# Kernel tuning notes

Hardware: AMD Instinct MI355X
Metric: run time of the kernel (lower is better)

## Reference

```python
import jax, jax.numpy as jnp
import numpy as np

NEG_SLOPE = 0.3

def capped_lrelu(x):
    # clamp(LeakyReLU_0.3(x), max=1)
    return jnp.minimum(jnp.where(x >= 0, x, NEG_SLOPE * x), 1.0)

def setup_inputs() -> dict:
    key = jax.random.key(0)
    ks = jax.random.split(key, 8)
    B, T, V, H, O = 64, 512, 512, 256, 512
    s = 1.0 / np.sqrt(H)
    return {
        "sentence": jax.random.normal(ks[0], (B, T, V), dtype=jnp.float32),
        "prev_state": jnp.zeros((1, B, H), dtype=jnp.float32),
        "W_ih": jax.random.normal(ks[1], (H, V), dtype=jnp.float32) * s,
        "b_ih": jax.random.normal(ks[2], (H,), dtype=jnp.float32) * s,
        "W_hh": jax.random.normal(ks[3], (H, H), dtype=jnp.float32) * s,
        "b_hh": jax.random.normal(ks[4], (H,), dtype=jnp.float32) * s,
        "W_out": jax.random.normal(ks[5], (O, H), dtype=jnp.float32) * s,
        "b_out": jax.random.normal(ks[6], (O,), dtype=jnp.float32) * s,
    }

def reference(sentence, prev_state, W_ih, b_ih, W_hh, b_hh, W_out, b_out):
    # nn.RNN(nonlinearity='relu'), batch_first, n_layers=1:
    #   h_t = relu(x_t @ W_ih^T + b_ih + h_{t-1} @ W_hh^T + b_hh)
    # Precompute input projections for all timesteps, scan the recurrence.
    x_proj = jnp.einsum('btv,hv->bth', sentence, W_ih) + b_ih  # [B,T,H]
    x_proj_t = jnp.swapaxes(x_proj, 0, 1)                      # [T,B,H]
    h0 = prev_state[0]                                         # [B,H]

    def step(h, xt):
        h_new = jax.nn.relu(xt + h @ W_hh.T + b_hh)
        return h_new, h_new

    h_last, out_seq = jax.lax.scan(step, h0, x_proj_t)         # [T,B,H]
    out_seq = jnp.swapaxes(out_seq, 0, 1)                      # [B,T,H]

    hidden_activ = capped_lrelu(out_seq)
    tags = jax.nn.sigmoid(jnp.einsum('bth,oh->bto', hidden_activ, W_out) + b_out)
    h_n = h_last[None]                                         # [1,B,H]
    return tags, h_n
```

## Files before the change

kernel.cpp:

```cpp
#include <hip/hip_runtime.h>
#include <hip/hip_bf16.h>


typedef __attribute__((ext_vector_type(8))) _Float16 half8;
typedef __attribute__((ext_vector_type(4))) _Float16 half4;
typedef __attribute__((ext_vector_type(4))) float   floatx4;

__device__ __forceinline__ void lds_barrier() {
    asm volatile("s_waitcnt lgkmcnt(0)\n\ts_barrier" ::: "memory");
}

__global__ void conv_f32_f16(const float* __restrict__ in, _Float16* __restrict__ out, int n4) {
    int idx = blockIdx.x * blockDim.x + threadIdx.x;
    if (idx >= n4) return;
    float4 v = ((const float4*)in)[idx];
    half4 h = { (_Float16)v.x, (_Float16)v.y, (_Float16)v.z, (_Float16)v.w };
    ((half4*)out)[idx] = h;
}

__global__ __launch_bounds__(256) void gemm1_xproj(const float* __restrict__ A,
                                                   const _Float16* __restrict__ Bw,
                                                   const float* __restrict__ b_ih,
                                                   const float* __restrict__ b_hh,
                                                   float* __restrict__ C) {
    const int K = 512, N = 256;
    int wave = threadIdx.x >> 6;
    int lane = threadIdx.x & 63;
    int row  = lane & 15;
    int quad = lane >> 4;
    int m0 = blockIdx.x * 64 + wave * 16;

    floatx4 acc[16];
#pragma unroll
    for (int i = 0; i < 16; i++) acc[i] = (floatx4){0.f, 0.f, 0.f, 0.f};

    const float* pa = A + (size_t)(m0 + row) * K + quad * 8;
    for (int k0 = 0; k0 < K; k0 += 32) {
        float4 a0 = *(const float4*)(pa + k0);
        float4 a1 = *(const float4*)(pa + k0 + 4);
        half8 a = { (_Float16)a0.x, (_Float16)a0.y, (_Float16)a0.z, (_Float16)a0.w,
                    (_Float16)a1.x, (_Float16)a1.y, (_Float16)a1.z, (_Float16)a1.w };
#pragma unroll
        for (int nt = 0; nt < 16; nt++) {
            const _Float16* pb = Bw + (size_t)(nt * 16 + row) * K + quad * 8 + k0;
            half8 b = *(const half8*)pb;
            acc[nt] = __builtin_amdgcn_mfma_f32_16x16x32_f16(a, b, acc[nt], 0, 0, 0);
        }
    }
#pragma unroll
    for (int nt = 0; nt < 16; nt++) {
        int n = nt * 16 + row;
        float bn = b_ih[n] + b_hh[n];
#pragma unroll
        for (int r = 0; r < 4; r++) {
            int m = m0 + quad * 4 + r;
            C[(size_t)m * N + n] = acc[nt][r] + bn;
        }
    }
}

__global__ __launch_bounds__(512, 2) void rnn_recur(const float* __restrict__ xp,
                                                    const float* __restrict__ h0,
                                                    const float* __restrict__ W_hh,
                                                    _Float16* __restrict__ hid,
                                                    float* __restrict__ h_n) {
    const int Hh = 256, T = 512, LD = 264;
    int b0   = blockIdx.x * 16;
    int wave = threadIdx.x >> 6;
    int lane = threadIdx.x & 63;
    int c    = lane & 15;
    int q    = lane >> 4;

    half8 wf[2][8];
#pragma unroll
    for (int nt = 0; nt < 2; nt++) {
        int n = (wave * 2 + nt) * 16 + c;
        const float* wr = W_hh + (size_t)n * Hh + q * 8;
#pragma unroll
        for (int kt = 0; kt < 8; kt++) {
            float4 x0 = *(const float4*)(wr + kt * 32);
            float4 x1 = *(const float4*)(wr + kt * 32 + 4);
            wf[nt][kt] = (half8){ (_Float16)x0.x, (_Float16)x0.y, (_Float16)x0.z, (_Float16)x0.w,
                                  (_Float16)x1.x, (_Float16)x1.y, (_Float16)x1.z, (_Float16)x1.w };
        }
    }

    __shared__ _Float16 hb[2][16][LD];
    for (int idx = threadIdx.x; idx < 16 * 256; idx += 512) {
        int m = idx >> 8, k = idx & 255;
        hb[0][m][k] = (_Float16)h0[(size_t)(b0 + m) * Hh + k];
    }
    __syncthreads();

    const float* xpb = xp + (size_t)(b0 + c) * T * Hh;
    _Float16* hidb = hid + (size_t)(b0 + c) * T * Hh;

    int noff[2];
#pragma unroll
    for (int nt = 0; nt < 2; nt++) noff[nt] = (wave * 2 + nt) * 16 + q * 4;

    float4 xq0[2], xq1[2];
#pragma unroll
    for (int nt = 0; nt < 2; nt++) {
        xq0[nt] = *(const float4*)(xpb + (size_t)0 * Hh + noff[nt]);
        xq1[nt] = *(const float4*)(xpb + (size_t)1 * Hh + noff[nt]);
    }

    auto do_step = [&](int t, float4 (&xq)[2]) {
        const _Float16* hr = &hb[t & 1][0][0];
        floatx4 aA0 = {0.f,0.f,0.f,0.f}, aA1 = {0.f,0.f,0.f,0.f};
        floatx4 aB0 = {0.f,0.f,0.f,0.f}, aB1 = {0.f,0.f,0.f,0.f};
#pragma unroll
        for (int kt = 0; kt < 4; kt++) {
            half8 hfA = *(const half8*)(hr + c * LD + kt * 32 + q * 8);
            half8 hfB = *(const half8*)(hr + c * LD + (kt + 4) * 32 + q * 8);
            aA0 = __builtin_amdgcn_mfma_f32_16x16x32_f16(wf[0][kt],     hfA, aA0, 0, 0, 0);
            aB0 = __builtin_amdgcn_mfma_f32_16x16x32_f16(wf[0][kt + 4], hfB, aB0, 0, 0, 0);
            aA1 = __builtin_amdgcn_mfma_f32_16x16x32_f16(wf[1][kt],     hfA, aA1, 0, 0, 0);
            aB1 = __builtin_amdgcn_mfma_f32_16x16x32_f16(wf[1][kt + 4], hfB, aB1, 0, 0, 0);
        }
        floatx4 acc[2];
        acc[0] = aA0 + aB0;
        acc[1] = aA1 + aB1;

        _Float16* hw = &hb[(t + 1) & 1][0][0];
#pragma unroll
        for (int nt = 0; nt < 2; nt++) {
            float v0 = fmaxf(acc[nt][0] + xq[nt].x, 0.f);
            float v1 = fmaxf(acc[nt][1] + xq[nt].y, 0.f);
            float v2 = fmaxf(acc[nt][2] + xq[nt].z, 0.f);
            float v3 = fmaxf(acc[nt][3] + xq[nt].w, 0.f);
            half4 hv = { (_Float16)v0, (_Float16)v1, (_Float16)v2, (_Float16)v3 };
            *(half4*)(hw + c * LD + noff[nt]) = hv;
            half4 hc = { (_Float16)fminf(v0, 1.f), (_Float16)fminf(v1, 1.f),
                         (_Float16)fminf(v2, 1.f), (_Float16)fminf(v3, 1.f) };
            *(half4*)(hidb + (size_t)t * Hh + noff[nt]) = hc;
            if (t == T - 1) {
                float4 hn = { v0, v1, v2, v3 };
                *(float4*)(h_n + (size_t)(b0 + c) * Hh + noff[nt]) = hn;
            }
        }
        int tp = (t + 2 < T) ? t + 2 : T - 1;
#pragma unroll
        for (int nt = 0; nt < 2; nt++)
            xq[nt] = *(const float4*)(xpb + (size_t)tp * Hh + noff[nt]);

        lds_barrier();
    };

    for (int t = 0; t < T; t += 2) {
        do_step(t,     xq0);
        do_step(t + 1, xq1);
    }
}

__global__ __launch_bounds__(256) void gemm3_tags(const _Float16* __restrict__ A,
                                                  const _Float16* __restrict__ Bw,
                                                  const float* __restrict__ bias,
                                                  float* __restrict__ C) {
    const int K = 256, N = 512;
    int wave = threadIdx.x >> 6;
    int lane = threadIdx.x & 63;
    int row  = lane & 15;
    int quad = lane >> 4;
    int m0 = blockIdx.x * 64 + wave * 16;
    int n_base = blockIdx.y * 256;

    floatx4 acc[16];
#pragma unroll
    for (int i = 0; i < 16; i++) acc[i] = (floatx4){0.f, 0.f, 0.f, 0.f};

    const _Float16* pa = A + (size_t)(m0 + row) * K + quad * 8;
    for (int k0 = 0; k0 < K; k0 += 32) {
        half8 a = *(const half8*)(pa + k0);
#pragma unroll
        for (int nt = 0; nt < 16; nt++) {
            const _Float16* pb = Bw + (size_t)(n_base + nt * 16 + row) * K + quad * 8 + k0;
            half8 b = *(const half8*)pb;
            acc[nt] = __builtin_amdgcn_mfma_f32_16x16x32_f16(a, b, acc[nt], 0, 0, 0);
        }
    }
#pragma unroll
    for (int nt = 0; nt < 16; nt++) {
        int n = n_base + nt * 16 + row;
        float bn = bias[n];
#pragma unroll
        for (int r = 0; r < 4; r++) {
            int m = m0 + quad * 4 + r;
            float v = acc[nt][r] + bn;
            C[(size_t)m * N + n] = 1.f / (1.f + __expf(-v));
        }
    }
}

extern "C" void kernel_launch(void* const* d_in, const int* in_sizes, int n_in,
                              void* d_out, int out_size, void* d_ws, size_t ws_size,
                              hipStream_t stream) {
    const float* sentence   = (const float*)d_in[0];
    const float* prev_state = (const float*)d_in[1];
    const float* W_ih       = (const float*)d_in[2];
    const float* b_ih       = (const float*)d_in[3];
    const float* W_hh       = (const float*)d_in[4];
    const float* b_hh       = (const float*)d_in[5];
    const float* W_out      = (const float*)d_in[6];
    const float* b_out      = (const float*)d_in[7];

    const size_t WIH_N   = 256u * 512u;
    const size_t WOUT_N  = 512u * 256u;
    const size_t XPROJ_N = 32768u * 256u;
    const size_t HID_N   = 64u * 512u * 256u;

    char* w = (char*)d_ws;
    _Float16* wih_f  = (_Float16*)w;  w += WIH_N * sizeof(_Float16);
    _Float16* wout_f = (_Float16*)w;  w += WOUT_N * sizeof(_Float16);
    float*    xproj  = (float*)w;     w += XPROJ_N * sizeof(float);
    _Float16* hid_f  = (_Float16*)w;  w += HID_N * sizeof(_Float16);

    float* tags = (float*)d_out;
    float* h_n  = (float*)d_out + 16777216;

    conv_f32_f16<<<(int)(WIH_N / 4 / 256),  256, 0, stream>>>(W_ih,  wih_f,  (int)(WIH_N / 4));
    conv_f32_f16<<<(int)(WOUT_N / 4 / 256), 256, 0, stream>>>(W_out, wout_f, (int)(WOUT_N / 4));

    gemm1_xproj<<<512, 256, 0, stream>>>(sentence, wih_f, b_ih, b_hh, xproj);

    rnn_recur<<<4, 512, 0, stream>>>(xproj, prev_state, W_hh, hid_f, h_n);

    gemm3_tags<<<dim3(512, 2), 256, 0, stream>>>(hid_f, wout_f, b_out, tags);
}
```

Before: 621.2 us.

## Fuse input GEMM, recurrence and output GEMM into one persistent kernel with flags

Replaces the three separate kernels with one persistent kernel of 256 blocks. Four blocks run the serial recurrence while the rest compute the input projection in time-chunk order and then the output projection. Global atomic flags let the recurrence start once its first time chunk is ready, and let the output GEMM start on finished chunks while the recurrence continues. This is meant to hide most of the two GEMMs behind the latency-bound recurrence. In exchange it adds spin-wait polling, a flag memset, and a risk of deadlock or contention if the 256 blocks are not all co-resident.

Result: slower. 1.621 ms (+160.9%).

```diff
diff --git a/kernel.cpp b/kernel.cpp
--- a/kernel.cpp
+++ b/kernel.cpp
@@ -8,6 +8,14 @@
 
 __device__ __forceinline__ void lds_barrier() {
     asm volatile("s_waitcnt lgkmcnt(0)\n\ts_barrier" ::: "memory");
+}
+
+__device__ __forceinline__ void wait_ge(int* p, int need) {
+    int spin = 0;
+    while (__hip_atomic_load(p, __ATOMIC_ACQUIRE, __HIP_MEMORY_SCOPE_AGENT) < need) {
+        __builtin_amdgcn_s_sleep(8);
+        if (++spin > (1 << 22)) break;
+    }
 }
 
 __global__ void conv_f32_f16(const float* __restrict__ in, _Float16* __restrict__ out, int n4) {
@@ -18,177 +26,210 @@
     ((half4*)out)[idx] = h;
 }
 
-__global__ __launch_bounds__(256) void gemm1_xproj(const float* __restrict__ A,
-                                                   const _Float16* __restrict__ Bw,
-                                                   const float* __restrict__ b_ih,
-                                                   const float* __restrict__ b_hh,
-                                                   float* __restrict__ C) {
-    const int K = 512, N = 256;
-    int wave = threadIdx.x >> 6;
-    int lane = threadIdx.x & 63;
-    int row  = lane & 15;
-    int quad = lane >> 4;
-    int m0 = blockIdx.x * 64 + wave * 16;
-
-    floatx4 acc[16];
-#pragma unroll
-    for (int i = 0; i < 16; i++) acc[i] = (floatx4){0.f, 0.f, 0.f, 0.f};
-
-    const float* pa = A + (size_t)(m0 + row) * K + quad * 8;
-    for (int k0 = 0; k0 < K; k0 += 32) {
-        float4 a0 = *(const float4*)(pa + k0);
-        float4 a1 = *(const float4*)(pa + k0 + 4);
-        half8 a = { (_Float16)a0.x, (_Float16)a0.y, (_Float16)a0.z, (_Float16)a0.w,
-                    (_Float16)a1.x, (_Float16)a1.y, (_Float16)a1.z, (_Float16)a1.w };
-#pragma unroll
-        for (int nt = 0; nt < 16; nt++) {
-            const _Float16* pb = Bw + (size_t)(nt * 16 + row) * K + quad * 8 + k0;
-            half8 b = *(const half8*)pb;
-            acc[nt] = __builtin_amdgcn_mfma_f32_16x16x32_f16(a, b, acc[nt], 0, 0, 0);
-        }
-    }
-#pragma unroll
-    for (int nt = 0; nt < 16; nt++) {
-        int n = nt * 16 + row;
-        float bn = b_ih[n] + b_hh[n];
-#pragma unroll
-        for (int r = 0; r < 4; r++) {
-            int m = m0 + quad * 4 + r;
-            C[(size_t)m * N + n] = acc[nt][r] + bn;
-        }
-    }
-}
-
-__global__ __launch_bounds__(512, 2) void rnn_recur(const float* __restrict__ xp,
-                                                    const float* __restrict__ h0,
-                                                    const float* __restrict__ W_hh,
-                                                    _Float16* __restrict__ hid,
-                                                    float* __restrict__ h_n) {
-    const int Hh = 256, T = 512, LD = 264;
-    int b0   = blockIdx.x * 16;
-    int wave = threadIdx.x >> 6;
-    int lane = threadIdx.x & 63;
-    int c    = lane & 15;
-    int q    = lane >> 4;
-
-    half8 wf[2][8];
-#pragma unroll
-    for (int nt = 0; nt < 2; nt++) {
-        int n = (wave * 2 + nt) * 16 + c;
-        const float* wr = W_hh + (size_t)n * Hh + q * 8;
-#pragma unroll
-        for (int kt = 0; kt < 8; kt++) {
-            float4 x0 = *(const float4*)(wr + kt * 32);
-            float4 x1 = *(const float4*)(wr + kt * 32 + 4);
-            wf[nt][kt] = (half8){ (_Float16)x0.x, (_Float16)x0.y, (_Float16)x0.z, (_Float16)x0.w,
-                                  (_Float16)x1.x, (_Float16)x1.y, (_Float16)x1.z, (_Float16)x1.w };
-        }
-    }
-
-    __shared__ _Float16 hb[2][16][LD];
-    for (int idx = threadIdx.x; idx < 16 * 256; idx += 512) {
-        int m = idx >> 8, k = idx & 255;
-        hb[0][m][k] = (_Float16)h0[(size_t)(b0 + m) * Hh + k];
-    }
-    __syncthreads();
-
-    const float* xpb = xp + (size_t)(b0 + c) * T * Hh;
-    _Float16* hidb = hid + (size_t)(b0 + c) * T * Hh;
-
-    int noff[2];
-#pragma unroll
-    for (int nt = 0; nt < 2; nt++) noff[nt] = (wave * 2 + nt) * 16 + q * 4;
-
-    float4 xq0[2], xq1[2];
-#pragma unroll
-    for (int nt = 0; nt < 2; nt++) {
-        xq0[nt] = *(const float4*)(xpb + (size_t)0 * Hh + noff[nt]);
-        xq1[nt] = *(const float4*)(xpb + (size_t)1 * Hh + noff[nt]);
-    }
-
-    auto do_step = [&](int t, float4 (&xq)[2]) {
-        const _Float16* hr = &hb[t & 1][0][0];
-        floatx4 aA0 = {0.f,0.f,0.f,0.f}, aA1 = {0.f,0.f,0.f,0.f};
-        floatx4 aB0 = {0.f,0.f,0.f,0.f}, aB1 = {0.f,0.f,0.f,0.f};
-#pragma unroll
-        for (int kt = 0; kt < 4; kt++) {
-            half8 hfA = *(const half8*)(hr + c * LD + kt * 32 + q * 8);
-            half8 hfB = *(const half8*)(hr + c * LD + (kt + 4) * 32 + q * 8);
-            aA0 = __builtin_amdgcn_mfma_f32_16x16x32_f16(wf[0][kt],     hfA, aA0, 0, 0, 0);
-            aB0 = __builtin_amdgcn_mfma_f32_16x16x32_f16(wf[0][kt + 4], hfB, aB0, 0, 0, 0);
-            aA1 = __builtin_amdgcn_mfma_f32_16x16x32_f16(wf[1][kt],     hfA, aA1, 0, 0, 0);
-            aB1 = __builtin_amdgcn_mfma_f32_16x16x32_f16(wf[1][kt + 4], hfB, aB1, 0, 0, 0);
-        }
-        floatx4 acc[2];
-        acc[0] = aA0 + aB0;
-        acc[1] = aA1 + aB1;
-
-        _Float16* hw = &hb[(t + 1) & 1][0][0];
+__global__ __launch_bounds__(512, 2) void mega(
+    const float* __restrict__ sentence,
+    const _Float16* __restrict__ wih,
+    const float* __restrict__ b_ih,
+    const float* __restrict__ b_hh,
+    float* __restrict__ xproj,
+    const float* __restrict__ h0g,
+    const float* __restrict__ W_hh,
+    _Float16* __restrict__ hid,
+    float* __restrict__ h_n,
+    const _Float16* __restrict__ wout,
+    const float* __restrict__ b_out,
+    float* __restrict__ tags,
+    int* __restrict__ flags)
+{
+    int* g1done  = flags;
+    int* rnnprog = flags + 32;
+
+    const int wave = threadIdx.x >> 6;
+    const int lane = threadIdx.x & 63;
+    const int row  = lane & 15;
+    const int quad = lane >> 4;
+
+    __shared__ _Float16 hb[2][16][264];
+
+    if (blockIdx.x < 4) {
+        const int Hh = 256, T = 512, LD = 264;
+        int b0 = blockIdx.x * 16;
+        int c = row;
+        int q = quad;
+
+        half8 wf[2][8];
 #pragma unroll
         for (int nt = 0; nt < 2; nt++) {
-            float v0 = fmaxf(acc[nt][0] + xq[nt].x, 0.f);
-            float v1 = fmaxf(acc[nt][1] + xq[nt].y, 0.f);
-            float v2 = fmaxf(acc[nt][2] + xq[nt].z, 0.f);
-            float v3 = fmaxf(acc[nt][3] + xq[nt].w, 0.f);
-            half4 hv = { (_Float16)v0, (_Float16)v1, (_Float16)v2, (_Float16)v3 };
-            *(half4*)(hw + c * LD + noff[nt]) = hv;
-            half4 hc = { (_Float16)fminf(v0, 1.f), (_Float16)fminf(v1, 1.f),
-                         (_Float16)fminf(v2, 1.f), (_Float16)fminf(v3, 1.f) };
-            *(half4*)(hidb + (size_t)t * Hh + noff[nt]) = hc;
-            if (t == T - 1) {
-                float4 hn = { v0, v1, v2, v3 };
-                *(float4*)(h_n + (size_t)(b0 + c) * Hh + noff[nt]) = hn;
-            }
-        }
-        int tp = (t + 2 < T) ? t + 2 : T - 1;
-#pragma unroll
-        for (int nt = 0; nt < 2; nt++)
-            xq[nt] = *(const float4*)(xpb + (size_t)tp * Hh + noff[nt]);
-
-        lds_barrier();
-    };
-
-    for (int t = 0; t < T; t += 2) {
-        do_step(t,     xq0);
-        do_step(t + 1, xq1);
-    }
-}
-
-__global__ __launch_bounds__(256) void gemm3_tags(const _Float16* __restrict__ A,
-                                                  const _Float16* __restrict__ Bw,
-                                                  const float* __restrict__ bias,
-                                                  float* __restrict__ C) {
-    const int K = 256, N = 512;
-    int wave = threadIdx.x >> 6;
-    int lane = threadIdx.x & 63;
-    int row  = lane & 15;
-    int quad = lane >> 4;
-    int m0 = blockIdx.x * 64 + wave * 16;
-    int n_base = blockIdx.y * 256;
-
-    floatx4 acc[16];
-#pragma unroll
-    for (int i = 0; i < 16; i++) acc[i] = (floatx4){0.f, 0.f, 0.f, 0.f};
-
-    const _Float16* pa = A + (size_t)(m0 + row) * K + quad * 8;
-    for (int k0 = 0; k0 < K; k0 += 32) {
-        half8 a = *(const half8*)(pa + k0);
-#pragma unroll
-        for (int nt = 0; nt < 16; nt++) {
-            const _Float16* pb = Bw + (size_t)(n_base + nt * 16 + row) * K + quad * 8 + k0;
-            half8 b = *(const half8*)pb;
-            acc[nt] = __builtin_amdgcn_mfma_f32_16x16x32_f16(a, b, acc[nt], 0, 0, 0);
-        }
-    }
-#pragma unroll
-    for (int nt = 0; nt < 16; nt++) {
-        int n = n_base + nt * 16 + row;
-        float bn = bias[n];
-#pragma unroll
-        for (int r = 0; r < 4; r++) {
-            int m = m0 + quad * 4 + r;
-            float v = acc[nt][r] + bn;
-            C[(size_t)m * N + n] = 1.f / (1.f + __expf(-v));
+            int n = (wave * 2 + nt) * 16 + c;
+            const float* wr = W_hh + (size_t)n * Hh + q * 8;
+#pragma unroll
+            for (int kt = 0; kt < 8; kt++) {
+                float4 x0 = *(const float4*)(wr + kt * 32);
+                float4 x1 = *(const float4*)(wr + kt * 32 + 4);
+                wf[nt][kt] = (half8){ (_Float16)x0.x, (_Float16)x0.y, (_Float16)x0.z, (_Float16)x0.w,
+                                      (_Float16)x1.x, (_Float16)x1.y, (_Float16)x1.z, (_Float16)x1.w };
+            }
+        }
+
+        for (int idx = threadIdx.x; idx < 16 * 256; idx += 512) {
+            int m = idx >> 8, k = idx & 255;
+            hb[0][m][k] = (_Float16)h0g[(size_t)(b0 + m) * Hh + k];
+        }
+        if (threadIdx.x == 0) wait_ge(&g1done[0], 64);
+        __syncthreads();
+
+        const float* xpb = xproj + (size_t)(b0 + c) * T * Hh;
+        _Float16* hidb = hid + (size_t)(b0 + c) * T * Hh;
+
+        int noff[2];
+#pragma unroll
+        for (int nt = 0; nt < 2; nt++) noff[nt] = (wave * 2 + nt) * 16 + q * 4;
+
+        float4 xq0[2], xq1[2];
+#pragma unroll
+        for (int nt = 0; nt < 2; nt++) {
+            xq0[nt] = *(const float4*)(xpb + (size_t)0 * Hh + noff[nt]);
+            xq1[nt] = *(const float4*)(xpb + (size_t)1 * Hh + noff[nt]);
+        }
+
+        auto do_step = [&](int t, float4 (&xq)[2]) {
+            const _Float16* hr = &hb[t & 1][0][0];
+            floatx4 aA0 = {0.f,0.f,0.f,0.f}, aA1 = {0.f,0.f,0.f,0.f};
+            floatx4 aB0 = {0.f,0.f,0.f,0.f}, aB1 = {0.f,0.f,0.f,0.f};
+#pragma unroll
+            for (int kt = 0; kt < 4; kt++) {
+                half8 hfA = *(const half8*)(hr + c * LD + kt * 32 + q * 8);
+                half8 hfB = *(const half8*)(hr + c * LD + (kt + 4) * 32 + q * 8);
+                aA0 = __builtin_amdgcn_mfma_f32_16x16x32_f16(wf[0][kt],     hfA, aA0, 0, 0, 0);
+                aB0 = __builtin_amdgcn_mfma_f32_16x16x32_f16(wf[0][kt + 4], hfB, aB0, 0, 0, 0);
+                aA1 = __builtin_amdgcn_mfma_f32_16x16x32_f16(wf[1][kt],     hfA, aA1, 0, 0, 0);
+                aB1 = __builtin_amdgcn_mfma_f32_16x16x32_f16(wf[1][kt + 4], hfB, aB1, 0, 0, 0);
+            }
+            floatx4 acc[2];
+            acc[0] = aA0 + aB0;
+            acc[1] = aA1 + aB1;
+
+            _Float16* hw = &hb[(t + 1) & 1][0][0];
+#pragma unroll
+            for (int nt = 0; nt < 2; nt++) {
+                float v0 = fmaxf(acc[nt][0] + xq[nt].x, 0.f);
+                float v1 = fmaxf(acc[nt][1] + xq[nt].y, 0.f);
+                float v2 = fmaxf(acc[nt][2] + xq[nt].z, 0.f);
+                float v3 = fmaxf(acc[nt][3] + xq[nt].w, 0.f);
+                half4 hv = { (_Float16)v0, (_Float16)v1, (_Float16)v2, (_Float16)v3 };
+                *(half4*)(hw + c * LD + noff[nt]) = hv;
+                half4 hc = { (_Float16)fminf(v0, 1.f), (_Float16)fminf(v1, 1.f),
+                             (_Float16)fminf(v2, 1.f), (_Float16)fminf(v3, 1.f) };
+                *(half4*)(hidb + (size_t)t * Hh + noff[nt]) = hc;
+                if (t == T - 1) {
+                    float4 hn = { v0, v1, v2, v3 };
+                    *(float4*)(h_n + (size_t)(b0 + c) * Hh + noff[nt]) = hn;
+                }
+            }
+            int tp = (t + 2 < T) ? t + 2 : T - 1;
+            if ((tp & 126) == 0) {
+                if (threadIdx.x == 0) wait_ge(&g1done[tp >> 7], 64);
+                __syncthreads();
+            }
+#pragma unroll
+            for (int nt = 0; nt < 2; nt++)
+                xq[nt] = *(const float4*)(xpb + (size_t)tp * Hh + noff[nt]);
+
+            lds_barrier();
+        };
+
+        for (int t = 0; t < T; t += 2) {
+            do_step(t,     xq0);
+            do_step(t + 1, xq1);
+            if (((t + 2) & 127) == 0) {
+                __threadfence();
+                __syncthreads();
+                if (threadIdx.x == 0)
+                    __hip_atomic_store(&rnnprog[blockIdx.x], t + 2,
+                                       __ATOMIC_RELEASE, __HIP_MEMORY_SCOPE_AGENT);
+            }
+        }
+    } else {
+        int w = blockIdx.x - 4;
+
+        const int K1 = 512, N1 = 256;
+        for (int qq = w; qq < 256; qq += 252) {
+            int chunk = qq >> 6;
+            int item  = (qq & 63) * 4 + chunk;
+            int m0 = item * 128 + wave * 16;
+
+            floatx4 acc[16];
+#pragma unroll
+            for (int i = 0; i < 16; i++) acc[i] = (floatx4){0.f, 0.f, 0.f, 0.f};
+
+            const float* pa = sentence + (size_t)(m0 + row) * K1 + quad * 8;
+            for (int k0 = 0; k0 < K1; k0 += 32) {
+                float4 a0 = *(const float4*)(pa + k0);
+                float4 a1 = *(const float4*)(pa + k0 + 4);
+                half8 a = { (_Float16)a0.x, (_Float16)a0.y, (_Float16)a0.z, (_Float16)a0.w,
+                            (_Float16)a1.x, (_Float16)a1.y, (_Float16)a1.z, (_Float16)a1.w };
+#pragma unroll
+                for (int nt = 0; nt < 16; nt++) {
+                    const _Float16* pb = wih + (size_t)(nt * 16 + row) * K1 + quad * 8 + k0;
+                    half8 b = *(const half8*)pb;
+                    acc[nt] = __builtin_amdgcn_mfma_f32_16x16x32_f16(a, b, acc[nt], 0, 0, 0);
+                }
+            }
+#pragma unroll
+            for (int nt = 0; nt < 16; nt++) {
+                int n = nt * 16 + row;
+                float bn = b_ih[n] + b_hh[n];
+#pragma unroll
+                for (int r = 0; r < 4; r++) {
+                    int m = m0 + quad * 4 + r;
+                    xproj[(size_t)m * N1 + n] = acc[nt][r] + bn;
+                }
+            }
+            __threadfence();
+            __syncthreads();
+            if (threadIdx.x == 0)
+                __hip_atomic_fetch_add(&g1done[chunk], 1,
+                                       __ATOMIC_RELEASE, __HIP_MEMORY_SCOPE_AGENT);
+        }
+
+        const int K3 = 256, N3 = 512;
+        for (int j = w; j < 512; j += 252) {
+            int tc = j >> 7;
+            int rr = j & 127;
+            int bb = rr >> 1;
+            int nh = rr & 1;
+
+            if (threadIdx.x == 0) wait_ge(&rnnprog[bb >> 4], (tc + 1) * 128);
+            __syncthreads();
+
+            int m0 = bb * 512 + tc * 128 + wave * 16;
+            int n_base = nh * 256;
+
+            floatx4 acc[16];
+#pragma unroll
+            for (int i = 0; i < 16; i++) acc[i] = (floatx4){0.f, 0.f, 0.f, 0.f};
+
+            const _Float16* pa = hid + (size_t)(m0 + row) * K3 + quad * 8;
+            for (int k0 = 0; k0 < K3; k0 += 32) {
+                half8 a = *(const half8*)(pa + k0);
+#pragma unroll
+                for (int nt = 0; nt < 16; nt++) {
+                    const _Float16* pb = wout + (size_t)(n_base + nt * 16 + row) * K3 + quad * 8 + k0;
+                    half8 b = *(const half8*)pb;
+                    acc[nt] = __builtin_amdgcn_mfma_f32_16x16x32_f16(a, b, acc[nt], 0, 0, 0);
+                }
+            }
+#pragma unroll
+            for (int nt = 0; nt < 16; nt++) {
+                int n = n_base + nt * 16 + row;
+                float bn = b_out[n];
+#pragma unroll
+                for (int r = 0; r < 4; r++) {
+                    int m = m0 + quad * 4 + r;
+                    float v = acc[nt][r] + bn;
+                    tags[(size_t)m * N3 + n] = 1.f / (1.f + __expf(-v));
+                }
+            }
         }
     }
 }
@@ -215,16 +256,17 @@
     _Float16* wout_f = (_Float16*)w;  w += WOUT_N * sizeof(_Float16);
     float*    xproj  = (float*)w;     w += XPROJ_N * sizeof(float);
     _Float16* hid_f  = (_Float16*)w;  w += HID_N * sizeof(_Float16);
+    int*      flags  = (int*)w;       w += 256;
 
     float* tags = (float*)d_out;
     float* h_n  = (float*)d_out + 16777216;
 
+    hipMemsetAsync(flags, 0, 256, stream);
+
     conv_f32_f16<<<(int)(WIH_N / 4 / 256),  256, 0, stream>>>(W_ih,  wih_f,  (int)(WIH_N / 4));
     conv_f32_f16<<<(int)(WOUT_N / 4 / 256), 256, 0, stream>>>(W_out, wout_f, (int)(WOUT_N / 4));
 
-    gemm1_xproj<<<512, 256, 0, stream>>>(sentence, wih_f, b_ih, b_hh, xproj);
-
-    rnn_recur<<<4, 512, 0, stream>>>(xproj, prev_state, W_hh, hid_f, h_n);
-
-    gemm3_tags<<<dim3(512, 2), 256, 0, stream>>>(hid_f, wout_f, b_out, tags);
-}
+    mega<<<256, 512, 0, stream>>>(sentence, wih_f, b_ih, b_hh, xproj,
+                                  prev_state, W_hh, hid_f, h_n,
+                                  wout_f, b_out, tags, flags);
+}
```

## Stage GEMM weight tiles in swizzled LDS via direct global-to-LDS loads

Applied to the files above, without the earlier changes.

Both projection GEMMs now stage a 256x256 f16 weight tile into LDS using global_load_lds with an XOR swizzle, then read B fragments from LDS instead of re-reading them from global memory per wave. Blocks grow to 512 threads covering 128 rows, and the two weight conversion launches merge into one. The aim is to cut redundant global/L2 traffic for weights. In exchange, each block uses 128 KB of LDS, which limits occupancy, and the staging adds a synchronous load phase.

New measurement: 515.3 us. 1.21x faster.

```diff
diff --git a/kernel.cpp b/kernel.cpp
--- a/kernel.cpp
+++ b/kernel.cpp
@@ -10,41 +10,73 @@
     asm volatile("s_waitcnt lgkmcnt(0)\n\ts_barrier" ::: "memory");
 }
 
-__global__ void conv_f32_f16(const float* __restrict__ in, _Float16* __restrict__ out, int n4) {
+__global__ void conv_weights(const float* __restrict__ wih, const float* __restrict__ wout,
+                             _Float16* __restrict__ out) {
     int idx = blockIdx.x * blockDim.x + threadIdx.x;
-    if (idx >= n4) return;
-    float4 v = ((const float4*)in)[idx];
+    const float* src = (idx < 32768) ? wih : wout;
+    int j = idx & 32767;
+    float4 v = ((const float4*)src)[j];
     half4 h = { (_Float16)v.x, (_Float16)v.y, (_Float16)v.z, (_Float16)v.w };
     ((half4*)out)[idx] = h;
 }
 
-__global__ __launch_bounds__(256) void gemm1_xproj(const float* __restrict__ A,
-                                                   const _Float16* __restrict__ Bw,
-                                                   const float* __restrict__ b_ih,
-                                                   const float* __restrict__ b_hh,
-                                                   float* __restrict__ C) {
+__device__ __forceinline__ void stage_weights_swz(const _Float16* __restrict__ src,
+                                                  int rowStrideHalves,
+                                                  _Float16* lds) {
+    int wave = threadIdx.x >> 6;
+    int lane = threadIdx.x & 63;
+#pragma unroll
+    for (int j = 0; j < 16; j++) {
+        int Lb = j * 8192 + wave * 1024 + lane * 16;
+        int n  = Lb >> 9;
+        int c  = Lb & 511;
+        int cs = c ^ ((n & 7) << 4);
+        const _Float16* g = src + (size_t)n * rowStrideHalves + (cs >> 1);
+        _Float16* l = lds + (j * 8192 + wave * 1024) / 2;
+        __builtin_amdgcn_global_load_lds((const __attribute__((address_space(1))) void*)g,
+                                         (__attribute__((address_space(3))) void*)l,
+                                         16, 0, 0);
+    }
+    asm volatile("s_waitcnt vmcnt(0)" ::: "memory");
+    __syncthreads();
+}
+
+__global__ __launch_bounds__(512, 2) void gemm1_xproj(const float* __restrict__ A,
+                                                      const _Float16* __restrict__ Bw,
+                                                      const float* __restrict__ b_ih,
+                                                      const float* __restrict__ b_hh,
+                                                      float* __restrict__ C) {
     const int K = 512, N = 256;
+    __shared__ _Float16 ldsB[65536];
     int wave = threadIdx.x >> 6;
     int lane = threadIdx.x & 63;
     int row  = lane & 15;
     int quad = lane >> 4;
-    int m0 = blockIdx.x * 64 + wave * 16;
+    int m0 = blockIdx.x * 128 + wave * 16;
 
     floatx4 acc[16];
 #pragma unroll
     for (int i = 0; i < 16; i++) acc[i] = (floatx4){0.f, 0.f, 0.f, 0.f};
 
     const float* pa = A + (size_t)(m0 + row) * K + quad * 8;
-    for (int k0 = 0; k0 < K; k0 += 32) {
-        float4 a0 = *(const float4*)(pa + k0);
-        float4 a1 = *(const float4*)(pa + k0 + 4);
-        half8 a = { (_Float16)a0.x, (_Float16)a0.y, (_Float16)a0.z, (_Float16)a0.w,
-                    (_Float16)a1.x, (_Float16)a1.y, (_Float16)a1.z, (_Float16)a1.w };
-#pragma unroll
-        for (int nt = 0; nt < 16; nt++) {
-            const _Float16* pb = Bw + (size_t)(nt * 16 + row) * K + quad * 8 + k0;
-            half8 b = *(const half8*)pb;
-            acc[nt] = __builtin_amdgcn_mfma_f32_16x16x32_f16(a, b, acc[nt], 0, 0, 0);
+    const char* lb = (const char*)ldsB;
+
+    for (int h = 0; h < 2; h++) {
+        if (h) __syncthreads();
+        stage_weights_swz(Bw + h * 256, 512, ldsB);
+
+        for (int kk = 0; kk < 256; kk += 32) {
+            float4 a0 = *(const float4*)(pa + h * 256 + kk);
+            float4 a1 = *(const float4*)(pa + h * 256 + kk + 4);
+            half8 a = { (_Float16)a0.x, (_Float16)a0.y, (_Float16)a0.z, (_Float16)a0.w,
+                        (_Float16)a1.x, (_Float16)a1.y, (_Float16)a1.z, (_Float16)a1.w };
+#pragma unroll
+            for (int nt = 0; nt < 16; nt++) {
+                int n = nt * 16 + row;
+                int byte = n * 512 + ((quad * 16 + kk * 2) ^ ((n & 7) << 4));
+                half8 b = *(const half8*)(lb + byte);
+                acc[nt] = __builtin_amdgcn_mfma_f32_16x16x32_f16(a, b, acc[nt], 0, 0, 0);
+            }
         }
     }
 #pragma unroll
@@ -85,7 +117,7 @@
         }
     }
 
-    __shared__ _Float16 hb[2][16][LD];
+    __shared__ _Float16 hb[2][16][264];
     for (int idx = threadIdx.x; idx < 16 * 256; idx += 512) {
         int m = idx >> 8, k = idx & 255;
         hb[0][m][k] = (_Float16)h0[(size_t)(b0 + m) * Hh + k];
@@ -154,35 +186,41 @@
     }
 }
 
-__global__ __launch_bounds__(256) void gemm3_tags(const _Float16* __restrict__ A,
-                                                  const _Float16* __restrict__ Bw,
-                                                  const float* __restrict__ bias,
-                                                  float* __restrict__ C) {
+__global__ __launch_bounds__(512, 2) void gemm3_tags(const _Float16* __restrict__ A,
+                                                     const _Float16* __restrict__ Bw,
+                                                     const float* __restrict__ bias,
+                                                     float* __restrict__ C) {
     const int K = 256, N = 512;
+    __shared__ _Float16 ldsB[65536];
     int wave = threadIdx.x >> 6;
     int lane = threadIdx.x & 63;
     int row  = lane & 15;
     int quad = lane >> 4;
-    int m0 = blockIdx.x * 64 + wave * 16;
-    int n_base = blockIdx.y * 256;
+    int m0 = blockIdx.x * 128 + wave * 16;
+    int nb = blockIdx.y;
+
+    stage_weights_swz(Bw + (size_t)nb * 256 * K, K, ldsB);
 
     floatx4 acc[16];
 #pragma unroll
     for (int i = 0; i < 16; i++) acc[i] = (floatx4){0.f, 0.f, 0.f, 0.f};
 
     const _Float16* pa = A + (size_t)(m0 + row) * K + quad * 8;
-    for (int k0 = 0; k0 < K; k0 += 32) {
-        half8 a = *(const half8*)(pa + k0);
+    const char* lb = (const char*)ldsB;
+
+    for (int kk = 0; kk < 256; kk += 32) {
+        half8 a = *(const half8*)(pa + kk);
 #pragma unroll
         for (int nt = 0; nt < 16; nt++) {
-            const _Float16* pb = Bw + (size_t)(n_base + nt * 16 + row) * K + quad * 8 + k0;
-            half8 b = *(const half8*)pb;
+            int n = nt * 16 + row;
+            int byte = n * 512 + ((quad * 16 + kk * 2) ^ ((n & 7) << 4));
+            half8 b = *(const half8*)(lb + byte);
             acc[nt] = __builtin_amdgcn_mfma_f32_16x16x32_f16(a, b, acc[nt], 0, 0, 0);
         }
     }
 #pragma unroll
     for (int nt = 0; nt < 16; nt++) {
-        int n = n_base + nt * 16 + row;
+        int n = nb * 256 + nt * 16 + row;
         float bn = bias[n];
 #pragma unroll
         for (int r = 0; r < 4; r++) {
@@ -219,12 +257,11 @@
     float* tags = (float*)d_out;
     float* h_n  = (float*)d_out + 16777216;
 
-    conv_f32_f16<<<(int)(WIH_N / 4 / 256),  256, 0, stream>>>(W_ih,  wih_f,  (int)(WIH_N / 4));
-    conv_f32_f16<<<(int)(WOUT_N / 4 / 256), 256, 0, stream>>>(W_out, wout_f, (int)(WOUT_N / 4));
-
-    gemm1_xproj<<<512, 256, 0, stream>>>(sentence, wih_f, b_ih, b_hh, xproj);
+    conv_weights<<<256, 256, 0, stream>>>(W_ih, W_out, wih_f);
+
+    gemm1_xproj<<<256, 512, 0, stream>>>(sentence, wih_f, b_ih, b_hh, xproj);
 
     rnn_recur<<<4, 512, 0, stream>>>(xproj, prev_state, W_hh, hid_f, h_n);
 
-    gemm3_tags<<<dim3(512, 2), 256, 0, stream>>>(hid_f, wout_f, b_out, tags);
-}
+    gemm3_tags<<<dim3(256, 2), 512, 0, stream>>>(hid_f, wout_f, b_out, tags);
+}
```
